# Kernel optimization log

Measured on AMD Instinct MI355X. Metric: run time of the kernel, lower is better.

The kernel has to match this reference:

```python
import jax, jax.numpy as jnp
import numpy as np

N_NODES = 50000
N_EDGES = 800000
IN_FEATS = 256
OUT_FEATS = 64


def setup_inputs() -> dict:
    key = jax.random.key(0)
    k1, k2, k3, k4 = jax.random.split(key, 4)
    feat = jax.random.normal(k1, (N_NODES, IN_FEATS), dtype=jnp.float32)
    src = jax.random.randint(k2, (N_EDGES,), 0, N_NODES, dtype=jnp.int32)
    dst = jax.random.randint(k3, (N_EDGES,), 0, N_NODES, dtype=jnp.int32)
    # Glorot-uniform like DGL's GraphConv weight init
    limit = float(np.sqrt(6.0 / (IN_FEATS + OUT_FEATS)))
    W = jax.random.uniform(k4, (IN_FEATS, OUT_FEATS), dtype=jnp.float32,
                           minval=-limit, maxval=limit)
    b = jnp.zeros((OUT_FEATS,), dtype=jnp.float32)
    return {"feat": feat, "src": src, "dst": dst, "W": W, "b": b}


def reference(feat, src, dst, W, b):
    n = feat.shape[0]
    ones = jnp.ones_like(src, dtype=feat.dtype)
    out_deg = jax.ops.segment_sum(ones, src, num_segments=n)
    in_deg = jax.ops.segment_sum(ones, dst, num_segments=n)
    # norm='both': deg^{-1/2}, degrees clamped to min 1 (allow_zero_in_degree)
    norm_src = jax.lax.rsqrt(jnp.maximum(out_deg, 1.0))   # [N]
    norm_dst = jax.lax.rsqrt(jnp.maximum(in_deg, 1.0))    # [N]
    # in_feats > out_feats -> apply weight before aggregation (DGL fast path)
    h = (feat * norm_src[:, None]) @ W                    # [N, out]
    agg = jax.ops.segment_sum(h[src], dst, num_segments=n)  # SpMM: sum messages at dst
    rst = agg * norm_dst[:, None] + b
    return jax.nn.sigmoid(rst)
```

## Files before the change

kernel.cpp:

```cpp
#include <hip/hip_runtime.h>
#include <hip/hip_bf16.h>
#include <math.h>

#define N_NODES 50000
#define N_EDGES 800000
#define IN_F 256
#define OUT_F 64

#define BKT 128
#define NB 391
#define CAP 3072
#define PARTA_BLOCKS 400
#define EPB (N_EDGES / PARTA_BLOCKS)
#define GEMM_BM 32
#define GEMM_BLOCKS 782
#define HIST_CHUNK 12500
#define HIST_BLOCKS 64

typedef __attribute__((ext_vector_type(8))) short bf16x8;
typedef __attribute__((ext_vector_type(4))) float f32x4;

__device__ __forceinline__ ushort f2bf(float x) {
    __hip_bfloat16 b = __float2bfloat16(x);
    return *reinterpret_cast<ushort*>(&b);
}
__device__ __forceinline__ float bf_lo(uint v) { return __uint_as_float(v << 16); }
__device__ __forceinline__ float bf_hi(uint v) { return __uint_as_float(v & 0xffff0000u); }

__global__ __launch_bounds__(256) void prep_kernel(int* __restrict__ bcntD,
                                                   const float* __restrict__ W,
                                                   ushort* __restrict__ Wpk,
                                                   int4* __restrict__ outdeg4) {
    const int tid = threadIdx.x;
    if (blockIdx.x == 0) {
        for (int i = tid; i < NB; i += 256) bcntD[i] = 0;
    } else if (blockIdx.x < 9) {
        const int gid = (blockIdx.x - 1) * 256 + tid;
        const int lane = gid & 63;
        const int ct = (gid >> 6) & 3;
        const int step = gid >> 8;
        const int kg = lane >> 4;
        const int n = lane & 15;
        const float* base = W + (size_t)(step * 32 + kg * 8) * OUT_F + ct * 16 + n;
        union { ushort u[8]; uint4 v; } pk;
        #pragma unroll
        for (int j = 0; j < 8; ++j) pk.u[j] = f2bf(base[(size_t)j * OUT_F]);
        ((uint4*)Wpk)[gid] = pk.v;
    } else {
        const int i = (blockIdx.x - 9) * 256 + tid;
        if (i < N_NODES / 4) outdeg4[i] = (int4){0, 0, 0, 0};
    }
}

__global__ __launch_bounds__(512) void fused_kernel(const int* __restrict__ src,
                                                    const int* __restrict__ dst,
                                                    int* __restrict__ bcntD,
                                                    uint* __restrict__ pairsD,
                                                    int* __restrict__ outdeg,
                                                    const float* __restrict__ feat,
                                                    const ushort* __restrict__ Wpk,
                                                    ushort* __restrict__ h) {
    __shared__ __align__(16) char smem[65536];
    const int bi = blockIdx.x;
    const int tid = threadIdx.x;

    if (bi < 2 * PARTA_BLOCKS && (bi & 1)) {
        int2* ed    = (int2*)smem;
        uint* stgD  = (uint*)(smem + 16000);
        int* lcntD  = (int*)(smem + 24000);
        int* ldofD  = (int*)(smem + 26048);
        int* lbaseD = (int*)(smem + 28096);
        int* wtotD  = (int*)(smem + 30144);
        const int id = bi >> 1;
        const int n4 = EPB / 4;

        for (int i = tid; i < NB; i += 512) lcntD[i] = 0;
        __syncthreads();

        const int4* t4 = (const int4*)(dst + (size_t)id * EPB);
        const int4* s4 = (const int4*)(src + (size_t)id * EPB);
        for (int i = tid; i < n4; i += 512) {
            const int4 d = t4[i];
            const int4 s = s4[i];
            ed[4 * i + 0] = (int2){d.x, s.x};
            ed[4 * i + 1] = (int2){d.y, s.y};
            ed[4 * i + 2] = (int2){d.z, s.z};
            ed[4 * i + 3] = (int2){d.w, s.w};
            atomicAdd(&lcntD[d.x >> 7], 1);
            atomicAdd(&lcntD[d.y >> 7], 1);
            atomicAdd(&lcntD[d.z >> 7], 1);
            atomicAdd(&lcntD[d.w >> 7], 1);
        }
        __syncthreads();

        for (int i = tid; i < NB; i += 512) {
            const int cD = lcntD[i];
            lbaseD[i] = cD ? atomicAdd(&bcntD[i], cD) : 0;
        }
        __syncthreads();

        {
            const int lane = tid & 63;
            const int wave = tid >> 6;
            const int vD = (tid < NB) ? lcntD[tid] : 0;
            int iD = vD;
            #pragma unroll
            for (int d = 1; d < 64; d <<= 1) {
                const int uD = __shfl_up(iD, d, 64);
                if (lane >= d) iD += uD;
            }
            if (lane == 63) wtotD[wave] = iD;
            __syncthreads();
            int woD = 0;
            #pragma unroll
            for (int w = 0; w < 8; ++w)
                if (w < wave) woD += wtotD[w];
            if (tid < NB) {
                ldofD[tid] = woD + iD - vD;
                lcntD[tid] = 0;
            }
        }
        __syncthreads();

        for (int i = tid; i < EPB; i += 512) {
            const int2 e = ed[i];
            const int bx = e.x >> 7;
            const int pos = atomicAdd(&lcntD[bx], 1);
            stgD[ldofD[bx] + pos] =
                ((uint)bx << 23) | ((uint)(e.x & 127) << 16) | (uint)e.y;
        }
        __syncthreads();

        for (int i = tid; i < EPB; i += 512) {
            const uint pv = stgD[i];
            const int bD = (int)(pv >> 23);
            pairsD[(size_t)bD * CAP + lbaseD[bD] + (i - ldofD[bD])] = pv & 0x7FFFFFu;
        }
    } else if (bi >= 2 * PARTA_BLOCKS && bi < 2 * PARTA_BLOCKS + 2 * HIST_BLOCKS
               && (bi & 1)) {
        int* cnt = (int*)smem;
        const int id = (bi - 2 * PARTA_BLOCKS) >> 1;
        const int chunk = id >> 4;
        const int slice = id & 15;
        const int base = chunk * HIST_CHUNK;

        for (int i = tid; i < HIST_CHUNK; i += 512) cnt[i] = 0;
        __syncthreads();

        const int4* s4 = (const int4*)(src + (size_t)slice * (N_EDGES / 16));
        for (int i = tid; i < (N_EDGES / 16) / 4; i += 512) {
            const int4 v = s4[i];
            int r;
            r = v.x - base; if ((unsigned)r < (unsigned)HIST_CHUNK) atomicAdd(&cnt[r], 1);
            r = v.y - base; if ((unsigned)r < (unsigned)HIST_CHUNK) atomicAdd(&cnt[r], 1);
            r = v.z - base; if ((unsigned)r < (unsigned)HIST_CHUNK) atomicAdd(&cnt[r], 1);
            r = v.w - base; if ((unsigned)r < (unsigned)HIST_CHUNK) atomicAdd(&cnt[r], 1);
        }
        __syncthreads();

        for (int i = tid; i < HIST_CHUNK; i += 512) {
            const int c = cnt[i];
            if (c) atomicAdd(&outdeg[base + i], c);
        }
    } else {
        const int id = (bi < 2 * PARTA_BLOCKS) ? (bi >> 1)
                     : (bi < 2 * PARTA_BLOCKS + 2 * HIST_BLOCKS)
                         ? (PARTA_BLOCKS + ((bi - 2 * PARTA_BLOCKS) >> 1))
                         : (bi - PARTA_BLOCKS - HIST_BLOCKS);
        const int half = tid >> 8;
        const int t = tid & 255;
        const int lane = t & 63;
        const int wave = t >> 6;
        const int m = lane & 15;
        const int g = lane >> 4;
        const int rowBase = (id * 2 + half) * GEMM_BM;
        float* ftile = (float*)(smem + (size_t)half * 32768);
        const char* fb = (const char*)feat;

        #pragma unroll
        for (int it = 0; it < 8; ++it) {
            const int R = it * 4 + wave;
            const int off = (lane * 16) ^ ((R & 7) << 4);
            int grow = rowBase + R;
            if (grow >= N_NODES) grow = N_NODES - 1;
            __builtin_amdgcn_global_load_lds(
                (const __attribute__((address_space(1))) void*)(fb + ((size_t)grow << 10) + off),
                (__attribute__((address_space(3))) void*)((char*)ftile + it * 4096 + wave * 1024),
                16, 0, 0);
        }
        __syncthreads();

        const int rowHalf = wave & 1;
        const int colHalf = wave >> 1;

        f32x4 acc[2];
        acc[0] = (f32x4){0.f, 0.f, 0.f, 0.f};
        acc[1] = (f32x4){0.f, 0.f, 0.f, 0.f};

        const int Rr = rowHalf * 16 + m;
        const int swz = (Rr & 7) << 4;
        const char* rowb = (const char*)ftile + (Rr << 10);
        const bf16x8* wp = (const bf16x8*)Wpk;

        #pragma unroll
        for (int step = 0; step < 8; ++step) {
            const int kb = step * 128 + g * 32;
            const float4 a0 = *(const float4*)(rowb + (kb ^ swz));
            const float4 a1 = *(const float4*)(rowb + ((kb + 16) ^ swz));
            bf16x8 aa;
            aa[0] = (short)f2bf(a0.x); aa[1] = (short)f2bf(a0.y);
            aa[2] = (short)f2bf(a0.z); aa[3] = (short)f2bf(a0.w);
            aa[4] = (short)f2bf(a1.x); aa[5] = (short)f2bf(a1.y);
            aa[6] = (short)f2bf(a1.z); aa[7] = (short)f2bf(a1.w);
            #pragma unroll
            for (int ct = 0; ct < 2; ++ct)
                acc[ct] = __builtin_amdgcn_mfma_f32_16x16x32_bf16(
                    aa, wp[(step * 4 + colHalf * 2 + ct) * 64 + lane], acc[ct], 0, 0, 0);
        }

        #pragma unroll
        for (int j = 0; j < 4; ++j) {
            const int row = rowBase + rowHalf * 16 + g * 4 + j;
            if (row < N_NODES) {
                #pragma unroll
                for (int ct = 0; ct < 2; ++ct)
                    h[(size_t)row * OUT_F + colHalf * 32 + ct * 16 + m] = f2bf(acc[ct][j]);
            }
        }
    }
}

__global__ __launch_bounds__(1024) void bucket_kernel(const int* __restrict__ outdeg,
                                                      float* __restrict__ normS,
                                                      const uint* __restrict__ pairsD,
                                                      const int* __restrict__ bcntD,
                                                      uint* __restrict__ ptrdeg,
                                                      ushort* __restrict__ sorted_src) {
    __shared__ int cnt[BKT];
    __shared__ int loff[BKT];
    __shared__ int wtot[2];
    const int bb = blockIdx.x;
    const int tid = threadIdx.x;
    const int node = bb * BKT + tid;

    if (tid < BKT) {
        cnt[tid] = 0;
        if (node < N_NODES)
            normS[node] = rsqrtf(fmaxf((float)outdeg[node], 1.0f));
    }
    __syncthreads();
    const int nD = bcntD[bb];
    const uint* pb = pairsD + (size_t)bb * CAP;
    for (int i = tid; i < nD; i += 1024) atomicAdd(&cnt[(pb[i] >> 16) & 127u], 1);
    __syncthreads();

    if (tid < BKT) {
        const int lane = tid & 63;
        const int wave = tid >> 6;
        const int v = cnt[tid];
        int incl = v;
        #pragma unroll
        for (int d = 1; d < 64; d <<= 1) {
            int u = __shfl_up(incl, d, 64);
            if (lane >= d) incl += u;
        }
        if (lane == 63) wtot[wave] = incl;
        loff[tid] = incl - v;
    }
    __syncthreads();
    if (tid < BKT) {
        const int wave = tid >> 6;
        const int ex = ((wave == 1) ? wtot[0] : 0) + loff[tid];
        loff[tid] = ex;
        const int v = cnt[tid];
        cnt[tid] = 0;
        if (node < N_NODES)
            ptrdeg[node] = (uint)(bb * CAP + ex) | ((uint)v << 21);
    }
    __syncthreads();

    for (int i = tid; i < nD; i += 1024) {
        const uint p = pb[i];
        const int local = (int)((p >> 16) & 127u);
        const int pos = atomicAdd(&cnt[local], 1);
        sorted_src[(size_t)bb * CAP + loff[local] + pos] = (ushort)(p & 0xFFFFu);
    }
}

__global__ __launch_bounds__(256) void gather_kernel(const uint* __restrict__ ptrdeg,
                                                     const ushort* __restrict__ sorted_src,
                                                     const float* __restrict__ normS,
                                                     const ushort* __restrict__ h,
                                                     const float* __restrict__ b,
                                                     float* __restrict__ out) {
    const int lane = threadIdx.x & 63;
    const int q = lane & 15;
    const int g = lane >> 4;
    int nid = (int)((blockIdx.x * (size_t)blockDim.x + threadIdx.x) >> 6);
    if (nid >= N_NODES) return;
    nid = __builtin_amdgcn_readfirstlane(nid);

    const uint pd = ptrdeg[nid];
    const int beg = (int)(pd & 0x1FFFFFu);
    const int deg = (int)(pd >> 21);

    float a0 = 0.f, a1 = 0.f, a2 = 0.f, a3 = 0.f;
    const int nfull = deg >> 2;
    int e = beg + g;
    #pragma unroll 4
    for (int i = 0; i < nfull; ++i) {
        const int s = (int)sorted_src[e];
        e += 4;
        const float ns = normS[s];
        const uint2 v = *(const uint2*)(h + (size_t)s * OUT_F + q * 4);
        a0 = fmaf(ns, bf_lo(v.x), a0); a1 = fmaf(ns, bf_hi(v.x), a1);
        a2 = fmaf(ns, bf_lo(v.y), a2); a3 = fmaf(ns, bf_hi(v.y), a3);
    }
    const int rem = deg & 3;
    if (g < rem) {
        const int s = (int)sorted_src[beg + (deg & ~3) + g];
        const float ns = normS[s];
        const uint2 v = *(const uint2*)(h + (size_t)s * OUT_F + q * 4);
        a0 = fmaf(ns, bf_lo(v.x), a0); a1 = fmaf(ns, bf_hi(v.x), a1);
        a2 = fmaf(ns, bf_lo(v.y), a2); a3 = fmaf(ns, bf_hi(v.y), a3);
    }
    a0 += __shfl_xor(a0, 16, 64); a1 += __shfl_xor(a1, 16, 64);
    a2 += __shfl_xor(a2, 16, 64); a3 += __shfl_xor(a3, 16, 64);
    a0 += __shfl_xor(a0, 32, 64); a1 += __shfl_xor(a1, 32, 64);
    a2 += __shfl_xor(a2, 32, 64); a3 += __shfl_xor(a3, 32, 64);

    if (g == 0) {
        const float norm = rsqrtf(fmaxf((float)deg, 1.0f));
        const float4 bb = *(const float4*)(b + q * 4);
        float4 o;
        o.x = 1.0f / (1.0f + expf(-(a0 * norm + bb.x)));
        o.y = 1.0f / (1.0f + expf(-(a1 * norm + bb.y)));
        o.z = 1.0f / (1.0f + expf(-(a2 * norm + bb.z)));
        o.w = 1.0f / (1.0f + expf(-(a3 * norm + bb.w)));
        *(float4*)(out + (size_t)nid * OUT_F + q * 4) = o;
    }
}

extern "C" void kernel_launch(void* const* d_in, const int* in_sizes, int n_in,
                              void* d_out, int out_size, void* d_ws, size_t ws_size,
                              hipStream_t stream) {
    const float* feat = (const float*)d_in[0];
    const int* src    = (const int*)d_in[1];
    const int* dst    = (const int*)d_in[2];
    const float* W    = (const float*)d_in[3];
    const float* b    = (const float*)d_in[4];
    float* out = (float*)d_out;

    char* ws = (char*)d_ws;
    size_t off = 0;
    ushort* h = (ushort*)(ws + off);        off += (size_t)N_NODES * OUT_F * 2;
    float* normS = (float*)(ws + off);      off += (size_t)N_NODES * 4;
    uint* ptrdeg = (uint*)(ws + off);       off += (size_t)N_NODES * 4;
    int* outdeg = (int*)(ws + off);         off += (size_t)N_NODES * 4;
    int* bcntD = (int*)(ws + off);          off += (size_t)NB * 4 + 16;
    ushort* Wpk = (ushort*)(ws + off);      off += (size_t)IN_F * OUT_F * 2;
    uint* pairsD = (uint*)(ws + off);       off += (size_t)NB * CAP * 4;
    ushort* sorted_src = (ushort*)(ws + off); off += (size_t)NB * CAP * 2;

    prep_kernel<<<9 + (N_NODES / 4 + 255) / 256, 256, 0, stream>>>(
        bcntD, W, Wpk, (int4*)outdeg);

    fused_kernel<<<PARTA_BLOCKS + HIST_BLOCKS + GEMM_BLOCKS, 512, 0, stream>>>(
        src, dst, bcntD, pairsD, outdeg, feat, Wpk, h);

    bucket_kernel<<<NB, 1024, 0, stream>>>(outdeg, normS,
                                           pairsD, bcntD, ptrdeg, sorted_src);

    gather_kernel<<<(N_NODES * 64 + 255) / 256, 256, 0, stream>>>(
        ptrdeg, sorted_src, normS, h, b, out);
}
```

Baseline: 67.49 us.

## Fuse bucket sort and gather into one kernel using LDS-resident sorted sources

Merges the per-bucket counting sort and the SpMM gather into a single kernel. The sorted source indices stay in shared memory instead of going to global memory, which removes one launch and the global write and read of sorted_src and ptrdeg. The source norm is now recomputed per edge from outdeg rather than read from a precomputed normS array. In exchange, the gather runs on only 391 blocks of 1024 threads with 16 waves each handling 8 nodes, so there is less parallelism and less latency hiding than the previous one-wave-per-node launch, and each edge pays an extra rsqrt.

```diff
diff --git a/kernel.cpp b/kernel.cpp
--- a/kernel.cpp
+++ b/kernel.cpp
@@ -230,24 +230,21 @@
     }
 }
 
-__global__ __launch_bounds__(1024) void bucket_kernel(const int* __restrict__ outdeg,
-                                                      float* __restrict__ normS,
-                                                      const uint* __restrict__ pairsD,
-                                                      const int* __restrict__ bcntD,
-                                                      uint* __restrict__ ptrdeg,
-                                                      ushort* __restrict__ sorted_src) {
+__global__ __launch_bounds__(1024) void buckgather_kernel(const int* __restrict__ outdeg,
+                                                          const uint* __restrict__ pairsD,
+                                                          const int* __restrict__ bcntD,
+                                                          const ushort* __restrict__ h,
+                                                          const float* __restrict__ b,
+                                                          float* __restrict__ out) {
+    __shared__ ushort sorted[CAP];
     __shared__ int cnt[BKT];
     __shared__ int loff[BKT];
+    __shared__ int degL[BKT];
     __shared__ int wtot[2];
     const int bb = blockIdx.x;
     const int tid = threadIdx.x;
-    const int node = bb * BKT + tid;
-
-    if (tid < BKT) {
-        cnt[tid] = 0;
-        if (node < N_NODES)
-            normS[node] = rsqrtf(fmaxf((float)outdeg[node], 1.0f));
-    }
+
+    if (tid < BKT) cnt[tid] = 0;
     __syncthreads();
     const int nD = bcntD[bb];
     const uint* pb = pairsD + (size_t)bb * CAP;
@@ -272,10 +269,8 @@
         const int wave = tid >> 6;
         const int ex = ((wave == 1) ? wtot[0] : 0) + loff[tid];
         loff[tid] = ex;
-        const int v = cnt[tid];
+        degL[tid] = cnt[tid];
         cnt[tid] = 0;
-        if (node < N_NODES)
-            ptrdeg[node] = (uint)(bb * CAP + ex) | ((uint)v << 21);
     }
     __syncthreads();
 
@@ -283,61 +278,57 @@
         const uint p = pb[i];
         const int local = (int)((p >> 16) & 127u);
         const int pos = atomicAdd(&cnt[local], 1);
-        sorted_src[(size_t)bb * CAP + loff[local] + pos] = (ushort)(p & 0xFFFFu);
-    }
-}
-
-__global__ __launch_bounds__(256) void gather_kernel(const uint* __restrict__ ptrdeg,
-                                                     const ushort* __restrict__ sorted_src,
-                                                     const float* __restrict__ normS,
-                                                     const ushort* __restrict__ h,
-                                                     const float* __restrict__ b,
-                                                     float* __restrict__ out) {
-    const int lane = threadIdx.x & 63;
+        sorted[loff[local] + pos] = (ushort)(p & 0xFFFFu);
+    }
+    __syncthreads();
+
+    const int lane = tid & 63;
+    const int waveId = tid >> 6;
     const int q = lane & 15;
     const int g = lane >> 4;
-    int nid = (int)((blockIdx.x * (size_t)blockDim.x + threadIdx.x) >> 6);
-    if (nid >= N_NODES) return;
-    nid = __builtin_amdgcn_readfirstlane(nid);
-
-    const uint pd = ptrdeg[nid];
-    const int beg = (int)(pd & 0x1FFFFFu);
-    const int deg = (int)(pd >> 21);
-
-    float a0 = 0.f, a1 = 0.f, a2 = 0.f, a3 = 0.f;
-    const int nfull = deg >> 2;
-    int e = beg + g;
-    #pragma unroll 4
-    for (int i = 0; i < nfull; ++i) {
-        const int s = (int)sorted_src[e];
-        e += 4;
-        const float ns = normS[s];
-        const uint2 v = *(const uint2*)(h + (size_t)s * OUT_F + q * 4);
-        a0 = fmaf(ns, bf_lo(v.x), a0); a1 = fmaf(ns, bf_hi(v.x), a1);
-        a2 = fmaf(ns, bf_lo(v.y), a2); a3 = fmaf(ns, bf_hi(v.y), a3);
-    }
-    const int rem = deg & 3;
-    if (g < rem) {
-        const int s = (int)sorted_src[beg + (deg & ~3) + g];
-        const float ns = normS[s];
-        const uint2 v = *(const uint2*)(h + (size_t)s * OUT_F + q * 4);
-        a0 = fmaf(ns, bf_lo(v.x), a0); a1 = fmaf(ns, bf_hi(v.x), a1);
-        a2 = fmaf(ns, bf_lo(v.y), a2); a3 = fmaf(ns, bf_hi(v.y), a3);
-    }
-    a0 += __shfl_xor(a0, 16, 64); a1 += __shfl_xor(a1, 16, 64);
-    a2 += __shfl_xor(a2, 16, 64); a3 += __shfl_xor(a3, 16, 64);
-    a0 += __shfl_xor(a0, 32, 64); a1 += __shfl_xor(a1, 32, 64);
-    a2 += __shfl_xor(a2, 32, 64); a3 += __shfl_xor(a3, 32, 64);
-
-    if (g == 0) {
-        const float norm = rsqrtf(fmaxf((float)deg, 1.0f));
-        const float4 bb = *(const float4*)(b + q * 4);
-        float4 o;
-        o.x = 1.0f / (1.0f + expf(-(a0 * norm + bb.x)));
-        o.y = 1.0f / (1.0f + expf(-(a1 * norm + bb.y)));
-        o.z = 1.0f / (1.0f + expf(-(a2 * norm + bb.z)));
-        o.w = 1.0f / (1.0f + expf(-(a3 * norm + bb.w)));
-        *(float4*)(out + (size_t)nid * OUT_F + q * 4) = o;
+
+    #pragma unroll
+    for (int i = 0; i < BKT / 16; ++i) {
+        const int local = i * 16 + waveId;
+        const int node = bb * BKT + local;
+        if (node >= N_NODES) continue;
+        const int beg = loff[local];
+        const int deg = degL[local];
+
+        float a0 = 0.f, a1 = 0.f, a2 = 0.f, a3 = 0.f;
+        const int nfull = deg >> 2;
+        int e = beg + g;
+        for (int it = 0; it < nfull; ++it) {
+            const int s = (int)sorted[e];
+            e += 4;
+            const float ns = rsqrtf(fmaxf((float)outdeg[s], 1.0f));
+            const uint2 v = *(const uint2*)(h + (size_t)s * OUT_F + q * 4);
+            a0 = fmaf(ns, bf_lo(v.x), a0); a1 = fmaf(ns, bf_hi(v.x), a1);
+            a2 = fmaf(ns, bf_lo(v.y), a2); a3 = fmaf(ns, bf_hi(v.y), a3);
+        }
+        const int rem = deg & 3;
+        if (g < rem) {
+            const int s = (int)sorted[beg + (deg & ~3) + g];
+            const float ns = rsqrtf(fmaxf((float)outdeg[s], 1.0f));
+            const uint2 v = *(const uint2*)(h + (size_t)s * OUT_F + q * 4);
+            a0 = fmaf(ns, bf_lo(v.x), a0); a1 = fmaf(ns, bf_hi(v.x), a1);
+            a2 = fmaf(ns, bf_lo(v.y), a2); a3 = fmaf(ns, bf_hi(v.y), a3);
+        }
+        a0 += __shfl_xor(a0, 16, 64); a1 += __shfl_xor(a1, 16, 64);
+        a2 += __shfl_xor(a2, 16, 64); a3 += __shfl_xor(a3, 16, 64);
+        a0 += __shfl_xor(a0, 32, 64); a1 += __shfl_xor(a1, 32, 64);
+        a2 += __shfl_xor(a2, 32, 64); a3 += __shfl_xor(a3, 32, 64);
+
+        if (g == 0) {
+            const float norm = rsqrtf(fmaxf((float)deg, 1.0f));
+            const float4 bb4 = *(const float4*)(b + q * 4);
+            float4 o;
+            o.x = 1.0f / (1.0f + expf(-(a0 * norm + bb4.x)));
+            o.y = 1.0f / (1.0f + expf(-(a1 * norm + bb4.y)));
+            o.z = 1.0f / (1.0f + expf(-(a2 * norm + bb4.z)));
+            o.w = 1.0f / (1.0f + expf(-(a3 * norm + bb4.w)));
+            *(float4*)(out + (size_t)node * OUT_F + q * 4) = o;
+        }
     }
 }
 
@@ -354,13 +345,10 @@
     char* ws = (char*)d_ws;
     size_t off = 0;
     ushort* h = (ushort*)(ws + off);        off += (size_t)N_NODES * OUT_F * 2;
-    float* normS = (float*)(ws + off);      off += (size_t)N_NODES * 4;
-    uint* ptrdeg = (uint*)(ws + off);       off += (size_t)N_NODES * 4;
     int* outdeg = (int*)(ws + off);         off += (size_t)N_NODES * 4;
     int* bcntD = (int*)(ws + off);          off += (size_t)NB * 4 + 16;
     ushort* Wpk = (ushort*)(ws + off);      off += (size_t)IN_F * OUT_F * 2;
     uint* pairsD = (uint*)(ws + off);       off += (size_t)NB * CAP * 4;
-    ushort* sorted_src = (ushort*)(ws + off); off += (size_t)NB * CAP * 2;
 
     prep_kernel<<<9 + (N_NODES / 4 + 255) / 256, 256, 0, stream>>>(
         bcntD, W, Wpk, (int4*)outdeg);
@@ -368,9 +356,5 @@
     fused_kernel<<<PARTA_BLOCKS + HIST_BLOCKS + GEMM_BLOCKS, 512, 0, stream>>>(
         src, dst, bcntD, pairsD, outdeg, feat, Wpk, h);
 
-    bucket_kernel<<<NB, 1024, 0, stream>>>(outdeg, normS,
-                                           pairsD, bcntD, ptrdeg, sorted_src);
-
-    gather_kernel<<<(N_NODES * 64 + 255) / 256, 256, 0, stream>>>(
-        ptrdeg, sorted_src, normS, h, b, out);
-}
+    buckgather_kernel<<<NB, 1024, 0, stream>>>(outdeg, pairsD, bcntD, h, b, out);
+}
```

Result: no change. 66.20 us (-1.9%).
